# Kernel tuning notes

Measured on AMD Instinct MI355X. Metric: run time of the kernel, lower is better.

## Reference

```python
import jax, jax.numpy as jnp
import numpy as np

N = 10000
E = 320000
DIN = 256
HID = 64
HEADS = 4
LAT = 32
NEG_SLOPE = 0.2


def _layer_params(key, din, heads, out_c):
    ks = jax.random.split(key, 6)
    s_in = 1.0 / np.sqrt(din)
    return dict(
        Wl=jax.random.normal(ks[0], (din, heads * out_c), jnp.float32) * s_in,
        bl=jnp.zeros((heads * out_c,), jnp.float32),
        Wr=jax.random.normal(ks[1], (din, heads * out_c), jnp.float32) * s_in,
        br=jnp.zeros((heads * out_c,), jnp.float32),
        att=jax.random.normal(ks[2], (heads, out_c), jnp.float32) * (1.0 / np.sqrt(out_c)),
        bo=jnp.zeros((heads * out_c,), jnp.float32),
    )


def setup_inputs() -> dict:
    key = jax.random.key(0)
    ks = jax.random.split(key, 8)
    inp = {
        "x": jax.random.normal(ks[0], (N, DIN), jnp.float32),
        "edge_index": jax.random.randint(ks[1], (2, E), 0, N, jnp.int64 if jax.config.jax_enable_x64 else jnp.int32),
        "eps": jax.random.normal(ks[2], (N, LAT), jnp.float32),
    }
    p0 = _layer_params(ks[3], DIN, HEADS, HID)
    p1 = _layer_params(ks[4], HID * HEADS, HEADS, HID)
    pmu = _layer_params(ks[5], HID * HEADS, 1, LAT)
    plv = _layer_params(ks[6], HID * HEADS, 1, LAT)
    for tag, p in (("l0", p0), ("l1", p1), ("mu", pmu), ("lv", plv)):
        for k, v in p.items():
            inp[f"{k}_{tag}"] = v
    return inp


def _gatv2(h, src, dst, Wl, bl, Wr, br, att, bo, heads, out_c, concat):
    # GATv2: e_ij = att . LeakyReLU(lin_l(x_j) + lin_r(x_i)), softmax over j for each i,
    # out_i = sum_j alpha_ij * lin_l(x_j). src = j (source), dst = i (target).
    xl = (h @ Wl + bl).reshape(-1, heads, out_c)  # [N,H,C]
    xr = (h @ Wr + br).reshape(-1, heads, out_c)
    e = jax.nn.leaky_relu(xl[src] + xr[dst], NEG_SLOPE)  # [E,H,C]
    score = jnp.einsum('ehc,hc->eh', e, att)             # [E,H]
    smax = jax.ops.segment_max(score, dst, num_segments=N)
    ex = jnp.exp(score - smax[dst])
    denom = jax.ops.segment_sum(ex, dst, num_segments=N)
    alpha = ex / (denom[dst] + 1e-16)                    # [E,H]
    out = jax.ops.segment_sum(alpha[:, :, None] * xl[src], dst, num_segments=N)  # [N,H,C]
    out = out.reshape(N, heads * out_c) if concat else out.mean(axis=1)
    return out + bo


def reference(x, edge_index, eps,
              Wl_l0, bl_l0, Wr_l0, br_l0, att_l0, bo_l0,
              Wl_l1, bl_l1, Wr_l1, br_l1, att_l1, bo_l1,
              Wl_mu, bl_mu, Wr_mu, br_mu, att_mu, bo_mu,
              Wl_lv, bl_lv, Wr_lv, br_lv, att_lv, bo_lv):
    loop = jnp.arange(N, dtype=edge_index.dtype)
    src = jnp.concatenate([edge_index[0], loop])  # add self-loops (PyG default)
    dst = jnp.concatenate([edge_index[1], loop])
    h = jax.nn.elu(_gatv2(x, src, dst, Wl_l0, bl_l0, Wr_l0, br_l0, att_l0, bo_l0, HEADS, HID, True))
    h = jax.nn.elu(_gatv2(h, src, dst, Wl_l1, bl_l1, Wr_l1, br_l1, att_l1, bo_l1, HEADS, HID, True))
    mu = _gatv2(h, src, dst, Wl_mu, bl_mu, Wr_mu, br_mu, att_mu, bo_mu, 1, LAT, False)
    log_var = _gatv2(h, src, dst, Wl_lv, bl_lv, Wr_lv, br_lv, att_lv, bo_lv, 1, LAT, False)
    z = mu + eps * jnp.exp(0.5 * log_var)  # reparameterize (training mode)
    adj_recon = z @ z.T                    # [N,N] dense decode
    return (adj_recon, mu, log_var)
```

## Files before the change

### kernel.cpp

```cpp
#include <hip/hip_runtime.h>
#include <hip/hip_bf16.h>
#include <math.h>

constexpr int Nn  = 10000;
constexpr int Ed  = 320000;
constexpr int DIN = 256;
constexpr float NEG = 0.2f;

constexpr size_t OFF_XL  = 0;
constexpr size_t OFF_XR  = 2560000;
constexpr size_t OFF_H   = 5120000;
constexpr size_t OFF_XSL = 7680000;
constexpr size_t OFF_XSR = 8320000;
constexpr size_t OFF_WLC = 8960000;
constexpr size_t OFF_WRC = 8976384;
constexpr size_t OFF_BLC = 8992768;
constexpr size_t OFF_BRC = 8992832;
constexpr size_t OFF_ATT = 8992896;
constexpr size_t OFF_BOC = 8992960;
constexpr size_t OFF_INT = 9000000;
constexpr int I_DEG = 0;
constexpr int I_ROW = 16384;
constexpr int I_CUR = 32768;
constexpr int I_CSR = 49152;
static_assert(OFF_INT + (I_CSR + Ed + Nn + 4) < 100000000, "scratch fits in adj region");

__device__ __forceinline__ unsigned short f2bf(float x) {
    unsigned int u = __float_as_uint(x);
    unsigned int r = (u + 0x7FFFu + ((u >> 16) & 1u)) >> 16;
    return (unsigned short)r;
}
__device__ __forceinline__ float bf2f(unsigned short b) {
    return __uint_as_float(((unsigned int)b) << 16);
}

typedef short bf16x8 __attribute__((ext_vector_type(8)));
typedef float f32x4  __attribute__((ext_vector_type(4)));

__global__ void k_init_deg(int* deg, int n) {
    int i = blockIdx.x * blockDim.x + threadIdx.x;
    if (i < n) deg[i] = 1;
}

__global__ void k_count(const int* __restrict__ dst, int* deg, int e) {
    int i = blockIdx.x * blockDim.x + threadIdx.x;
    if (i < e) atomicAdd(&deg[dst[i]], 1);
}

__global__ void k_scan(const int* __restrict__ deg, int* row_ptr, int* cursor, int n) {
    __shared__ int sums[256];
    int t = threadIdx.x;
    int chunk = (n + 255) / 256;
    int start = t * chunk, end = min(start + chunk, n);
    int s = 0;
    for (int i = start; i < end; ++i) s += deg[i];
    sums[t] = s;
    __syncthreads();
    for (int off = 1; off < 256; off <<= 1) {
        int v = (t >= off) ? sums[t - off] : 0;
        __syncthreads();
        sums[t] += v;
        __syncthreads();
    }
    int run = sums[t] - s;
    for (int i = start; i < end; ++i) { row_ptr[i] = run; cursor[i] = run; run += deg[i]; }
    if (t == 255) row_ptr[n] = sums[255];
}

__global__ void k_scatter(const int* __restrict__ src, const int* __restrict__ dst,
                          int* cursor, int* csr, int e, int n) {
    int i = blockIdx.x * blockDim.x + threadIdx.x;
    if (i < e) {
        int d = dst[i];
        int pos = atomicAdd(&cursor[d], 1);
        csr[pos] = src[i];
    } else if (i < e + n) {
        int v = i - e;
        int pos = atomicAdd(&cursor[v], 1);
        csr[pos] = v;
    }
}

template <typename OT>
__global__ __launch_bounds__(256) void k_gemm(const float* __restrict__ A,
                                              const float* __restrict__ W,
                                              const float* __restrict__ bias,
                                              OT* __restrict__ out,
                                              int M, int Ncols) {
    constexpr int K = 256;
    __shared__ float As[32][68];
    __shared__ float Ws[32][64];
    int tid = threadIdx.x;
    int tx = tid & 15, ty = tid >> 4;
    int m0 = blockIdx.x * 64, n0 = blockIdx.y * 64;
    float acc[4][4] = {};
    int am = tid >> 2, akb = (tid & 3) * 8;
    int wk = tid >> 3, wnb = (tid & 7) * 8;
    const bool arow_ok = (m0 + am) < M;
    const float* Aptr = A + (size_t)(m0 + am) * K + akb;
    const float* Wptr = W + (size_t)wk * Ncols + n0 + wnb;

    for (int k0 = 0; k0 < K; k0 += 32) {
        float4 a0 = {0, 0, 0, 0}, a1 = {0, 0, 0, 0};
        if (arow_ok) {
            a0 = *(const float4*)(Aptr + k0);
            a1 = *(const float4*)(Aptr + k0 + 4);
        }
        float4 w0 = *(const float4*)(Wptr + (size_t)k0 * Ncols);
        float4 w1 = *(const float4*)(Wptr + (size_t)k0 * Ncols + 4);
        __syncthreads();
        As[akb + 0][am] = a0.x; As[akb + 1][am] = a0.y; As[akb + 2][am] = a0.z; As[akb + 3][am] = a0.w;
        As[akb + 4][am] = a1.x; As[akb + 5][am] = a1.y; As[akb + 6][am] = a1.z; As[akb + 7][am] = a1.w;
        *(float4*)&Ws[wk][wnb] = w0;
        *(float4*)&Ws[wk][wnb + 4] = w1;
        __syncthreads();
        #pragma unroll
        for (int k = 0; k < 32; ++k) {
            float4 a = *(const float4*)&As[k][ty * 4];
            float4 b = *(const float4*)&Ws[k][tx * 4];
            float av[4] = {a.x, a.y, a.z, a.w};
            float bv[4] = {b.x, b.y, b.z, b.w};
            #pragma unroll
            for (int i2 = 0; i2 < 4; ++i2)
                #pragma unroll
                for (int j2 = 0; j2 < 4; ++j2)
                    acc[i2][j2] = fmaf(av[i2], bv[j2], acc[i2][j2]);
        }
    }
    #pragma unroll
    for (int i2 = 0; i2 < 4; ++i2) {
        int row = m0 + ty * 4 + i2;
        if (row < M) {
            int col = n0 + tx * 4;
            float o0 = acc[i2][0] + bias[col + 0];
            float o1 = acc[i2][1] + bias[col + 1];
            float o2 = acc[i2][2] + bias[col + 2];
            float o3 = acc[i2][3] + bias[col + 3];
            if constexpr (sizeof(OT) == 4) {
                float4 o = {o0, o1, o2, o3};
                *(float4*)&out[(size_t)row * Ncols + col] = o;
            } else {
                ushort4 s;
                s.x = f2bf(o0); s.y = f2bf(o1); s.z = f2bf(o2); s.w = f2bf(o3);
                *(ushort4*)&out[(size_t)row * Ncols + col] = s;
            }
        }
    }
}

__device__ __forceinline__ float lrelu(float x) { return x > 0.f ? x : NEG * x; }

template <bool DO_ELU>
__global__ __launch_bounds__(256) void k_gat4(const unsigned short* __restrict__ xl,
                                              const float* __restrict__ xr,
                                              const float* __restrict__ att,
                                              const float* __restrict__ bo,
                                              const int* __restrict__ row_ptr,
                                              const int* __restrict__ csr,
                                              float* __restrict__ out, int n) {
    int lane = threadIdx.x & 63;
    int node = (blockIdx.x * blockDim.x + threadIdx.x) >> 6;
    if (node >= n) return;
    int f = lane * 4;
    float4 xrr  = *(const float4*)&xr[(size_t)node * 256 + f];
    float4 attr = *(const float4*)&att[f];
    float m = -INFINITY, d = 0.f;
    float4 acc = {0.f, 0.f, 0.f, 0.f};

    int e0 = row_ptr[node], e1 = row_ptr[node + 1];
    int e = e0;
    for (; e + 1 < e1; e += 2) {
        int ja = csr[e], jb = csr[e + 1];
        ushort4 ua = *(const ushort4*)&xl[(size_t)ja * 256 + f];
        ushort4 ub = *(const ushort4*)&xl[(size_t)jb * 256 + f];
        float4 va = {bf2f(ua.x), bf2f(ua.y), bf2f(ua.z), bf2f(ua.w)};
        float4 vb = {bf2f(ub.x), bf2f(ub.y), bf2f(ub.z), bf2f(ub.w)};
        float ta = attr.x * lrelu(va.x + xrr.x) + attr.y * lrelu(va.y + xrr.y)
                 + attr.z * lrelu(va.z + xrr.z) + attr.w * lrelu(va.w + xrr.w);
        float tb = attr.x * lrelu(vb.x + xrr.x) + attr.y * lrelu(vb.y + xrr.y)
                 + attr.z * lrelu(vb.z + xrr.z) + attr.w * lrelu(vb.w + xrr.w);
        #pragma unroll
        for (int mask = 1; mask <= 8; mask <<= 1) {
            ta += __shfl_xor(ta, mask, 64);
            tb += __shfl_xor(tb, mask, 64);
        }
        float mn = fmaxf(m, fmaxf(ta, tb));
        float sc = __expf(m - mn);
        float pa = __expf(ta - mn), pb = __expf(tb - mn);
        d = d * sc + pa + pb;
        acc.x = acc.x * sc + pa * va.x + pb * vb.x;
        acc.y = acc.y * sc + pa * va.y + pb * vb.y;
        acc.z = acc.z * sc + pa * va.z + pb * vb.z;
        acc.w = acc.w * sc + pa * va.w + pb * vb.w;
        m = mn;
    }
    if (e < e1) {
        int j = csr[e];
        ushort4 u = *(const ushort4*)&xl[(size_t)j * 256 + f];
        float4 v = {bf2f(u.x), bf2f(u.y), bf2f(u.z), bf2f(u.w)};
        float t = attr.x * lrelu(v.x + xrr.x) + attr.y * lrelu(v.y + xrr.y)
                + attr.z * lrelu(v.z + xrr.z) + attr.w * lrelu(v.w + xrr.w);
        #pragma unroll
        for (int mask = 1; mask <= 8; mask <<= 1) t += __shfl_xor(t, mask, 64);
        float mn = fmaxf(m, t);
        float sc = __expf(m - mn), p = __expf(t - mn);
        d = d * sc + p;
        acc.x = acc.x * sc + p * v.x;
        acc.y = acc.y * sc + p * v.y;
        acc.z = acc.z * sc + p * v.z;
        acc.w = acc.w * sc + p * v.w;
        m = mn;
    }
    float inv = 1.f / (d + 1e-16f);
    float4 bo4 = *(const float4*)&bo[f];
    float4 o;
    o.x = acc.x * inv + bo4.x;
    o.y = acc.y * inv + bo4.y;
    o.z = acc.z * inv + bo4.z;
    o.w = acc.w * inv + bo4.w;
    if (DO_ELU) {
        o.x = o.x > 0.f ? o.x : expm1f(o.x);
        o.y = o.y > 0.f ? o.y : expm1f(o.y);
        o.z = o.z > 0.f ? o.z : expm1f(o.z);
        o.w = o.w > 0.f ? o.w : expm1f(o.w);
    }
    *(float4*)&out[(size_t)node * 256 + f] = o;
}

template <int H, int C, bool DO_ELU, bool SPLIT>
__global__ __launch_bounds__(256) void k_gat(const unsigned short* __restrict__ xl,
                                             const float* __restrict__ xr,
                                             const float* __restrict__ att,
                                             const float* __restrict__ bo,
                                             const int* __restrict__ row_ptr,
                                             const int* __restrict__ csr,
                                             float* __restrict__ out0,
                                             float* __restrict__ out1, int n) {
    constexpr int F = H * C;
    constexpr int R = F / 64;
    int lane = threadIdx.x & 63;
    int node = (blockIdx.x * blockDim.x + threadIdx.x) >> 6;
    if (node >= n) return;

    float xrr[R], attr[R], m[R], d[R], acc[R];
    #pragma unroll
    for (int r = 0; r < R; ++r) {
        xrr[r]  = xr[(size_t)node * F + r * 64 + lane];
        attr[r] = att[r * 64 + lane];
        m[r] = -INFINITY;
        d[r] = 0.f;
        acc[r] = 0.f;
    }
    int e0 = row_ptr[node], e1 = row_ptr[node + 1];
    for (int e = e0; e < e1; ++e) {
        int j = csr[e];
        float v[R], s[R];
        #pragma unroll
        for (int r = 0; r < R; ++r) {
            v[r] = bf2f(xl[(size_t)j * F + r * 64 + lane]);
            float t = v[r] + xrr[r];
            t = (t > 0.f) ? t : NEG * t;
            t *= attr[r];
            #pragma unroll
            for (int mask = C / 2; mask >= 1; mask >>= 1)
                t += __shfl_xor(t, mask, 64);
            s[r] = t;
        }
        #pragma unroll
        for (int r = 0; r < R; ++r) {
            if (s[r] > m[r]) {
                float sc = __expf(m[r] - s[r]);
                d[r] *= sc; acc[r] *= sc; m[r] = s[r];
            }
            float p = __expf(s[r] - m[r]);
            d[r] += p;
            acc[r] = fmaf(p, v[r], acc[r]);
        }
    }
    #pragma unroll
    for (int r = 0; r < R; ++r) {
        float o = acc[r] / (d[r] + 1e-16f) + bo[r * 64 + lane];
        if (DO_ELU) o = (o > 0.f) ? o : expm1f(o);
        if (SPLIT) {
            int f = r * 64 + lane;
            int h = f / C, c = f % C;
            float* op = (h == 0) ? out0 : out1;
            op[(size_t)node * C + c] = o;
        } else {
            out0[(size_t)node * F + r * 64 + lane] = o;
        }
    }
}

__global__ void k_cat(const float* __restrict__ Wlmu, const float* __restrict__ Wllv,
                      const float* __restrict__ Wrmu, const float* __restrict__ Wrlv,
                      const float* __restrict__ blmu, const float* __restrict__ bllv,
                      const float* __restrict__ brmu, const float* __restrict__ brlv,
                      const float* __restrict__ attmu, const float* __restrict__ attlv,
                      const float* __restrict__ bomu, const float* __restrict__ bolv,
                      float* WLC, float* WRC, float* BLC, float* BRC, float* ATTC, float* BOC) {
    int i = blockIdx.x * blockDim.x + threadIdx.x;
    if (i < 256 * 64) {
        int k = i >> 6, c = i & 63;
        WLC[i] = (c < 32) ? Wlmu[k * 32 + c] : Wllv[k * 32 + c - 32];
        WRC[i] = (c < 32) ? Wrmu[k * 32 + c] : Wrlv[k * 32 + c - 32];
    }
    if (i < 64) {
        BLC[i]  = (i < 32) ? blmu[i]  : bllv[i - 32];
        BRC[i]  = (i < 32) ? brmu[i]  : brlv[i - 32];
        ATTC[i] = (i < 32) ? attmu[i] : attlv[i - 32];
        BOC[i]  = (i < 32) ? bomu[i]  : bolv[i - 32];
    }
}

__global__ void k_z2(const float* __restrict__ mu, const float* __restrict__ lv,
                     const float* __restrict__ eps,
                     unsigned short* __restrict__ zhi,
                     unsigned short* __restrict__ zlo, int n) {
    int i = blockIdx.x * blockDim.x + threadIdx.x;
    if (i < n * 8) {
        float4 m4 = ((const float4*)mu)[i];
        float4 l4 = ((const float4*)lv)[i];
        float4 e4 = ((const float4*)eps)[i];
        float zv[4];
        zv[0] = m4.x + e4.x * __expf(0.5f * l4.x);
        zv[1] = m4.y + e4.y * __expf(0.5f * l4.y);
        zv[2] = m4.z + e4.z * __expf(0.5f * l4.z);
        zv[3] = m4.w + e4.w * __expf(0.5f * l4.w);
        ushort4 h, lo;
        h.x = f2bf(zv[0]); lo.x = f2bf(zv[0] - bf2f(h.x));
        h.y = f2bf(zv[1]); lo.y = f2bf(zv[1] - bf2f(h.y));
        h.z = f2bf(zv[2]); lo.z = f2bf(zv[2] - bf2f(h.z));
        h.w = f2bf(zv[3]); lo.w = f2bf(zv[3] - bf2f(h.w));
        *(ushort4*)&zhi[(size_t)i * 4] = h;
        *(ushort4*)&zlo[(size_t)i * 4] = lo;
    }
}

constexpr int JTM = 25;

__global__ __launch_bounds__(256) void k_adjm(const unsigned short* __restrict__ zhi,
                                              const unsigned short* __restrict__ zlo,
                                              float* __restrict__ adj, int n) {
    int wave  = threadIdx.x >> 6;
    int l     = threadIdx.x & 63;
    int strip = blockIdx.y * 4 + wave;
    if (strip * 16 >= n) return;
    int i0   = strip * 16;
    int arow = i0 + (l & 15);
    int koff = (l >> 4) * 8;
    bf16x8 a_hi = *(const bf16x8*)(zhi + (size_t)arow * 32 + koff);
    bf16x8 a_lo = *(const bf16x8*)(zlo + (size_t)arow * 32 + koff);
    int crow = i0 + (l >> 4) * 4;

    for (int t = 0; t < JTM; ++t) {
        int j0   = (blockIdx.x * JTM + t) * 16;
        int brow = j0 + (l & 15);
        bf16x8 b_hi = *(const bf16x8*)(zhi + (size_t)brow * 32 + koff);
        bf16x8 b_lo = *(const bf16x8*)(zlo + (size_t)brow * 32 + koff);
        f32x4 acc = {0.f, 0.f, 0.f, 0.f};
        acc = __builtin_amdgcn_mfma_f32_16x16x32_bf16(a_hi, b_hi, acc, 0, 0, 0);
        acc = __builtin_amdgcn_mfma_f32_16x16x32_bf16(a_hi, b_lo, acc, 0, 0, 0);
        acc = __builtin_amdgcn_mfma_f32_16x16x32_bf16(a_lo, b_hi, acc, 0, 0, 0);
        size_t base = (size_t)crow * n + j0 + (l & 15);
        adj[base]                 = acc[0];
        adj[base + (size_t)n]     = acc[1];
        adj[base + (size_t)n * 2] = acc[2];
        adj[base + (size_t)n * 3] = acc[3];
    }
}

constexpr int JT = 8;
__global__ __launch_bounds__(256) void k_adj_fb(const float* __restrict__ mu,
                                                const float* __restrict__ lv,
                                                const float* __restrict__ eps,
                                                float* __restrict__ adj, int n) {
    __shared__ float Zi[32][68];
    __shared__ float Zj[32][68];
    int tid = threadIdx.x;
    int tx = tid & 15, ty = tid >> 4;
    int i0 = blockIdx.y * 64;
    int r = tid >> 2, kq = (tid & 3) * 8;

    auto load8 = [&](int row, float4& a, float4& b) {
        a = make_float4(0.f, 0.f, 0.f, 0.f);
        b = make_float4(0.f, 0.f, 0.f, 0.f);
        if (row < n) {
            float4 m0 = *(const float4*)&mu[row * 32 + kq];
            float4 l0 = *(const float4*)&lv[row * 32 + kq];
            float4 e0 = *(const float4*)&eps[row * 32 + kq];
            float4 m1 = *(const float4*)&mu[row * 32 + kq + 4];
            float4 l1 = *(const float4*)&lv[row * 32 + kq + 4];
            float4 e1 = *(const float4*)&eps[row * 32 + kq + 4];
            a.x = m0.x + e0.x * __expf(0.5f * l0.x);
            a.y = m0.y + e0.y * __expf(0.5f * l0.y);
            a.z = m0.z + e0.z * __expf(0.5f * l0.z);
            a.w = m0.w + e0.w * __expf(0.5f * l0.w);
            b.x = m1.x + e1.x * __expf(0.5f * l1.x);
            b.y = m1.y + e1.y * __expf(0.5f * l1.y);
            b.z = m1.z + e1.z * __expf(0.5f * l1.z);
            b.w = m1.w + e1.w * __expf(0.5f * l1.w);
        }
    };

    {
        float4 a, b;
        load8(i0 + r, a, b);
        Zi[kq + 0][r] = a.x; Zi[kq + 1][r] = a.y; Zi[kq + 2][r] = a.z; Zi[kq + 3][r] = a.w;
        Zi[kq + 4][r] = b.x; Zi[kq + 5][r] = b.y; Zi[kq + 6][r] = b.z; Zi[kq + 7][r] = b.w;
    }
    __syncthreads();
    float4 af[32];
    #pragma unroll
    for (int k = 0; k < 32; ++k) af[k] = *(const float4*)&Zi[k][ty * 4];

    for (int jt = 0; jt < JT; ++jt) {
        int j0 = (blockIdx.x * JT + jt) * 64;
        if (j0 >= n) break;
        {
            float4 a, b;
            load8(j0 + r, a, b);
            __syncthreads();
            Zj[kq + 0][r] = a.x; Zj[kq + 1][r] = a.y; Zj[kq + 2][r] = a.z; Zj[kq + 3][r] = a.w;
            Zj[kq + 4][r] = b.x; Zj[kq + 5][r] = b.y; Zj[kq + 6][r] = b.z; Zj[kq + 7][r] = b.w;
            __syncthreads();
        }
        float acc[4][4] = {};
        #pragma unroll
        for (int k = 0; k < 32; ++k) {
            float4 b = *(const float4*)&Zj[k][tx * 4];
            float av[4] = {af[k].x, af[k].y, af[k].z, af[k].w};
            float bv[4] = {b.x, b.y, b.z, b.w};
            #pragma unroll
            for (int i2 = 0; i2 < 4; ++i2)
                #pragma unroll
                for (int j2 = 0; j2 < 4; ++j2)
                    acc[i2][j2] = fmaf(av[i2], bv[j2], acc[i2][j2]);
        }
        int col = j0 + tx * 4;
        if (col < n) {
            #pragma unroll
            for (int i2 = 0; i2 < 4; ++i2) {
                int row = i0 + ty * 4 + i2;
                if (row < n) {
                    float4 o = {acc[i2][0], acc[i2][1], acc[i2][2], acc[i2][3]};
                    *(float4*)&adj[(size_t)row * n + col] = o;
                }
            }
        }
    }
}

extern "C" void kernel_launch(void* const* d_in, const int* in_sizes, int n_in,
                              void* d_out, int out_size, void* d_ws, size_t ws_size,
                              hipStream_t stream) {
    const float* x      = (const float*)d_in[0];
    const int*   edges  = (const int*)d_in[1];
    const float* eps    = (const float*)d_in[2];
    const float* Wl0 = (const float*)d_in[3];
    const float* bl0 = (const float*)d_in[4];
    const float* Wr0 = (const float*)d_in[5];
    const float* br0 = (const float*)d_in[6];
    const float* at0 = (const float*)d_in[7];
    const float* bo0 = (const float*)d_in[8];
    const float* Wl1 = (const float*)d_in[9];
    const float* bl1 = (const float*)d_in[10];
    const float* Wr1 = (const float*)d_in[11];
    const float* br1 = (const float*)d_in[12];
    const float* at1 = (const float*)d_in[13];
    const float* bo1 = (const float*)d_in[14];
    const float* Wlmu = (const float*)d_in[15];
    const float* blmu = (const float*)d_in[16];
    const float* Wrmu = (const float*)d_in[17];
    const float* brmu = (const float*)d_in[18];
    const float* atmu = (const float*)d_in[19];
    const float* bomu = (const float*)d_in[20];
    const float* Wllv = (const float*)d_in[21];
    const float* bllv = (const float*)d_in[22];
    const float* Wrlv = (const float*)d_in[23];
    const float* brlv = (const float*)d_in[24];
    const float* atlv = (const float*)d_in[25];
    const float* bolv = (const float*)d_in[26];

    float* base   = (float*)d_out;
    float* adj    = base;
    float* mu_out = base + (size_t)Nn * Nn;
    float* lv_out = mu_out + (size_t)Nn * 32;

    unsigned short* XLB  = (unsigned short*)(base + OFF_XL);
    float* XR  = base + OFF_XR;
    float* H   = base + OFF_H;
    unsigned short* XSLB = (unsigned short*)(base + OFF_XSL);
    float* XSR = base + OFF_XSR;
    float* WLC = base + OFF_WLC;
    float* WRC = base + OFF_WRC;
    float* BLC = base + OFF_BLC;
    float* BRC = base + OFF_BRC;
    float* ATT = base + OFF_ATT;
    float* BOC = base + OFF_BOC;
    int* ib  = (int*)(base + OFF_INT);
    int* deg = ib + I_DEG;
    int* row = ib + I_ROW;
    int* cur = ib + I_CUR;
    int* csr = ib + I_CSR;
    const int* srcp = edges;
    const int* dstp = edges + Ed;

    k_init_deg<<<(Nn + 255) / 256, 256, 0, stream>>>(deg, Nn);
    k_count<<<(Ed + 255) / 256, 256, 0, stream>>>(dstp, deg, Ed);
    k_scan<<<1, 256, 0, stream>>>(deg, row, cur, Nn);
    k_scatter<<<(Ed + Nn + 255) / 256, 256, 0, stream>>>(srcp, dstp, cur, csr, Ed, Nn);

    dim3 g4(157, 4), g1(157, 1);
    k_gemm<unsigned short><<<g4, 256, 0, stream>>>(x, Wl0, bl0, XLB, Nn, 256);
    k_gemm<float><<<g4, 256, 0, stream>>>(x, Wr0, br0, XR, Nn, 256);
    k_gat4<true><<<2500, 256, 0, stream>>>(XLB, XR, at0, bo0, row, csr, H, Nn);
    k_gemm<unsigned short><<<g4, 256, 0, stream>>>(H, Wl1, bl1, XLB, Nn, 256);
    k_gemm<float><<<g4, 256, 0, stream>>>(H, Wr1, br1, XR, Nn, 256);
    k_gat4<true><<<2500, 256, 0, stream>>>(XLB, XR, at1, bo1, row, csr, H, Nn);
    k_cat<<<64, 256, 0, stream>>>(Wlmu, Wllv, Wrmu, Wrlv, blmu, bllv, brmu, brlv,
                                  atmu, atlv, bomu, bolv, WLC, WRC, BLC, BRC, ATT, BOC);
    k_gemm<unsigned short><<<g1, 256, 0, stream>>>(H, WLC, BLC, XSLB, Nn, 64);
    k_gemm<float><<<g1, 256, 0, stream>>>(H, WRC, BRC, XSR, Nn, 64);
    k_gat<2, 32, false, true><<<2500, 256, 0, stream>>>(XSLB, XSR, ATT, BOC, row, csr, mu_out, lv_out, Nn);

    size_t need = (size_t)Nn * 32 * 2 * sizeof(unsigned short);
    if (ws_size >= need) {
        unsigned short* zhi = (unsigned short*)d_ws;
        unsigned short* zlo = zhi + (size_t)Nn * 32;
        k_z2<<<(Nn * 8 + 255) / 256, 256, 0, stream>>>(mu_out, lv_out, eps, zhi, zlo, Nn);
        dim3 ga(25, 157);
        k_adjm<<<ga, 256, 0, stream>>>(zhi, zlo, adj, Nn);
    } else {
        dim3 ga(20, 157);
        k_adj_fb<<<ga, 256, 0, stream>>>(mu_out, lv_out, eps, adj, Nn);
    }
}
```

Baseline: 431.6 us.

## Fuse lin_l/lin_r GEMMs per layer and fold reparameterization into final GAT

Merges the two separate GEMMs for lin_l and lin_r into one kernel that loads each A tile once and accumulates against both weight matrices. The z reparameterization (mu + eps*exp(0.5*logvar), split into bf16 hi/lo) is moved into the final GAT kernel, which removes the k_z2 launch and its re-read of mu and log_var. This saves repeated activation reads and three kernel launches, at the cost of double the register accumulators and more shared memory in the GEMM, which may reduce occupancy.

```diff
diff --git a/kernel.cpp b/kernel.cpp
--- a/kernel.cpp
+++ b/kernel.cpp
@@ -81,24 +81,29 @@
     }
 }
 
-template <typename OT>
-__global__ __launch_bounds__(256) void k_gemm(const float* __restrict__ A,
-                                              const float* __restrict__ W,
-                                              const float* __restrict__ bias,
-                                              OT* __restrict__ out,
-                                              int M, int Ncols) {
+template <int NC>
+__global__ __launch_bounds__(256) void k_gemm2(const float* __restrict__ A,
+                                               const float* __restrict__ WL,
+                                               const float* __restrict__ biasL,
+                                               unsigned short* __restrict__ outL,
+                                               const float* __restrict__ WR,
+                                               const float* __restrict__ biasR,
+                                               float* __restrict__ outR,
+                                               int M) {
     constexpr int K = 256;
     __shared__ float As[32][68];
-    __shared__ float Ws[32][64];
+    __shared__ float WsL[32][64];
+    __shared__ float WsR[32][64];
     int tid = threadIdx.x;
     int tx = tid & 15, ty = tid >> 4;
     int m0 = blockIdx.x * 64, n0 = blockIdx.y * 64;
-    float acc[4][4] = {};
+    float accL[4][4] = {}, accR[4][4] = {};
     int am = tid >> 2, akb = (tid & 3) * 8;
     int wk = tid >> 3, wnb = (tid & 7) * 8;
     const bool arow_ok = (m0 + am) < M;
-    const float* Aptr = A + (size_t)(m0 + am) * K + akb;
-    const float* Wptr = W + (size_t)wk * Ncols + n0 + wnb;
+    const float* Aptr  = A  + (size_t)(m0 + am) * K + akb;
+    const float* WLptr = WL + (size_t)wk * NC + n0 + wnb;
+    const float* WRptr = WR + (size_t)wk * NC + n0 + wnb;
 
     for (int k0 = 0; k0 < K; k0 += 32) {
         float4 a0 = {0, 0, 0, 0}, a1 = {0, 0, 0, 0};
@@ -106,25 +111,33 @@
             a0 = *(const float4*)(Aptr + k0);
             a1 = *(const float4*)(Aptr + k0 + 4);
         }
-        float4 w0 = *(const float4*)(Wptr + (size_t)k0 * Ncols);
-        float4 w1 = *(const float4*)(Wptr + (size_t)k0 * Ncols + 4);
+        float4 wl0 = *(const float4*)(WLptr + (size_t)k0 * NC);
+        float4 wl1 = *(const float4*)(WLptr + (size_t)k0 * NC + 4);
+        float4 wr0 = *(const float4*)(WRptr + (size_t)k0 * NC);
+        float4 wr1 = *(const float4*)(WRptr + (size_t)k0 * NC + 4);
         __syncthreads();
         As[akb + 0][am] = a0.x; As[akb + 1][am] = a0.y; As[akb + 2][am] = a0.z; As[akb + 3][am] = a0.w;
         As[akb + 4][am] = a1.x; As[akb + 5][am] = a1.y; As[akb + 6][am] = a1.z; As[akb + 7][am] = a1.w;
-        *(float4*)&Ws[wk][wnb] = w0;
-        *(float4*)&Ws[wk][wnb + 4] = w1;
+        *(float4*)&WsL[wk][wnb]     = wl0;
+        *(float4*)&WsL[wk][wnb + 4] = wl1;
+        *(float4*)&WsR[wk][wnb]     = wr0;
+        *(float4*)&WsR[wk][wnb + 4] = wr1;
         __syncthreads();
         #pragma unroll
         for (int k = 0; k < 32; ++k) {
-            float4 a = *(const float4*)&As[k][ty * 4];
-            float4 b = *(const float4*)&Ws[k][tx * 4];
-            float av[4] = {a.x, a.y, a.z, a.w};
-            float bv[4] = {b.x, b.y, b.z, b.w};
+            float4 a  = *(const float4*)&As[k][ty * 4];
+            float4 bl = *(const float4*)&WsL[k][tx * 4];
+            float4 br = *(const float4*)&WsR[k][tx * 4];
+            float av[4]  = {a.x, a.y, a.z, a.w};
+            float blv[4] = {bl.x, bl.y, bl.z, bl.w};
+            float brv[4] = {br.x, br.y, br.z, br.w};
             #pragma unroll
             for (int i2 = 0; i2 < 4; ++i2)
                 #pragma unroll
-                for (int j2 = 0; j2 < 4; ++j2)
-                    acc[i2][j2] = fmaf(av[i2], bv[j2], acc[i2][j2]);
+                for (int j2 = 0; j2 < 4; ++j2) {
+                    accL[i2][j2] = fmaf(av[i2], blv[j2], accL[i2][j2]);
+                    accR[i2][j2] = fmaf(av[i2], brv[j2], accR[i2][j2]);
+                }
         }
     }
     #pragma unroll
@@ -132,18 +145,18 @@
         int row = m0 + ty * 4 + i2;
         if (row < M) {
             int col = n0 + tx * 4;
-            float o0 = acc[i2][0] + bias[col + 0];
-            float o1 = acc[i2][1] + bias[col + 1];
-            float o2 = acc[i2][2] + bias[col + 2];
-            float o3 = acc[i2][3] + bias[col + 3];
-            if constexpr (sizeof(OT) == 4) {
-                float4 o = {o0, o1, o2, o3};
-                *(float4*)&out[(size_t)row * Ncols + col] = o;
-            } else {
-                ushort4 s;
-                s.x = f2bf(o0); s.y = f2bf(o1); s.z = f2bf(o2); s.w = f2bf(o3);
-                *(ushort4*)&out[(size_t)row * Ncols + col] = s;
-            }
+            ushort4 s;
+            s.x = f2bf(accL[i2][0] + biasL[col + 0]);
+            s.y = f2bf(accL[i2][1] + biasL[col + 1]);
+            s.z = f2bf(accL[i2][2] + biasL[col + 2]);
+            s.w = f2bf(accL[i2][3] + biasL[col + 3]);
+            *(ushort4*)&outL[(size_t)row * NC + col] = s;
+            float4 o;
+            o.x = accR[i2][0] + biasR[col + 0];
+            o.y = accR[i2][1] + biasR[col + 1];
+            o.z = accR[i2][2] + biasR[col + 2];
+            o.w = accR[i2][3] + biasR[col + 3];
+            *(float4*)&outR[(size_t)row * NC + col] = o;
         }
     }
 }
@@ -227,68 +240,54 @@
     *(float4*)&out[(size_t)node * 256 + f] = o;
 }
 
-template <int H, int C, bool DO_ELU, bool SPLIT>
-__global__ __launch_bounds__(256) void k_gat(const unsigned short* __restrict__ xl,
-                                             const float* __restrict__ xr,
-                                             const float* __restrict__ att,
-                                             const float* __restrict__ bo,
-                                             const int* __restrict__ row_ptr,
-                                             const int* __restrict__ csr,
-                                             float* __restrict__ out0,
-                                             float* __restrict__ out1, int n) {
-    constexpr int F = H * C;
-    constexpr int R = F / 64;
+__global__ __launch_bounds__(256) void k_gatz(const unsigned short* __restrict__ xl,
+                                              const float* __restrict__ xr,
+                                              const float* __restrict__ att,
+                                              const float* __restrict__ bo,
+                                              const int* __restrict__ row_ptr,
+                                              const int* __restrict__ csr,
+                                              const float* __restrict__ eps,
+                                              float* __restrict__ out0,
+                                              float* __restrict__ out1,
+                                              unsigned short* __restrict__ zhi,
+                                              unsigned short* __restrict__ zlo, int n) {
+    constexpr int C = 32;
     int lane = threadIdx.x & 63;
     int node = (blockIdx.x * blockDim.x + threadIdx.x) >> 6;
     if (node >= n) return;
 
-    float xrr[R], attr[R], m[R], d[R], acc[R];
-    #pragma unroll
-    for (int r = 0; r < R; ++r) {
-        xrr[r]  = xr[(size_t)node * F + r * 64 + lane];
-        attr[r] = att[r * 64 + lane];
-        m[r] = -INFINITY;
-        d[r] = 0.f;
-        acc[r] = 0.f;
-    }
+    float xrr  = xr[(size_t)node * 64 + lane];
+    float attr = att[lane];
+    float m = -INFINITY, d = 0.f, acc = 0.f;
+
     int e0 = row_ptr[node], e1 = row_ptr[node + 1];
     for (int e = e0; e < e1; ++e) {
         int j = csr[e];
-        float v[R], s[R];
+        float v = bf2f(xl[(size_t)j * 64 + lane]);
+        float t = v + xrr;
+        t = (t > 0.f) ? t : NEG * t;
+        t *= attr;
         #pragma unroll
-        for (int r = 0; r < R; ++r) {
-            v[r] = bf2f(xl[(size_t)j * F + r * 64 + lane]);
-            float t = v[r] + xrr[r];
-            t = (t > 0.f) ? t : NEG * t;
-            t *= attr[r];
-            #pragma unroll
-            for (int mask = C / 2; mask >= 1; mask >>= 1)
-                t += __shfl_xor(t, mask, 64);
-            s[r] = t;
-        }
-        #pragma unroll
-        for (int r = 0; r < R; ++r) {
-            if (s[r] > m[r]) {
-                float sc = __expf(m[r] - s[r]);
-                d[r] *= sc; acc[r] *= sc; m[r] = s[r];
-            }
-            float p = __expf(s[r] - m[r]);
-            d[r] += p;
-            acc[r] = fmaf(p, v[r], acc[r]);
-        }
-    }
-    #pragma unroll
-    for (int r = 0; r < R; ++r) {
-        float o = acc[r] / (d[r] + 1e-16f) + bo[r * 64 + lane];
-        if (DO_ELU) o = (o > 0.f) ? o : expm1f(o);
-        if (SPLIT) {
-            int f = r * 64 + lane;
-            int h = f / C, c = f % C;
-            float* op = (h == 0) ? out0 : out1;
-            op[(size_t)node * C + c] = o;
-        } else {
-            out0[(size_t)node * F + r * 64 + lane] = o;
-        }
+        for (int mask = C / 2; mask >= 1; mask >>= 1)
+            t += __shfl_xor(t, mask, 64);
+        if (t > m) {
+            float sc = __expf(m - t);
+            d *= sc; acc *= sc; m = t;
+        }
+        float p = __expf(t - m);
+        d += p;
+        acc = fmaf(p, v, acc);
+    }
+    float o = acc / (d + 1e-16f) + bo[lane];
+    int c = lane & 31;
+    float* op = (lane < 32) ? out0 : out1;
+    op[(size_t)node * C + c] = o;
+    float lvv = __shfl(o, lane + 32, 64);
+    if (zhi != nullptr && lane < 32) {
+        float zc = o + eps[(size_t)node * 32 + lane] * __expf(0.5f * lvv);
+        unsigned short h = f2bf(zc);
+        zhi[(size_t)node * 32 + lane] = h;
+        zlo[(size_t)node * 32 + lane] = f2bf(zc - bf2f(h));
     }
 }
 
@@ -310,30 +309,6 @@
         BRC[i]  = (i < 32) ? brmu[i]  : brlv[i - 32];
         ATTC[i] = (i < 32) ? attmu[i] : attlv[i - 32];
         BOC[i]  = (i < 32) ? bomu[i]  : bolv[i - 32];
-    }
-}
-
-__global__ void k_z2(const float* __restrict__ mu, const float* __restrict__ lv,
-                     const float* __restrict__ eps,
-                     unsigned short* __restrict__ zhi,
-                     unsigned short* __restrict__ zlo, int n) {
-    int i = blockIdx.x * blockDim.x + threadIdx.x;
-    if (i < n * 8) {
-        float4 m4 = ((const float4*)mu)[i];
-        float4 l4 = ((const float4*)lv)[i];
-        float4 e4 = ((const float4*)eps)[i];
-        float zv[4];
-        zv[0] = m4.x + e4.x * __expf(0.5f * l4.x);
-        zv[1] = m4.y + e4.y * __expf(0.5f * l4.y);
-        zv[2] = m4.z + e4.z * __expf(0.5f * l4.z);
-        zv[3] = m4.w + e4.w * __expf(0.5f * l4.w);
-        ushort4 h, lo;
-        h.x = f2bf(zv[0]); lo.x = f2bf(zv[0] - bf2f(h.x));
-        h.y = f2bf(zv[1]); lo.y = f2bf(zv[1] - bf2f(h.y));
-        h.z = f2bf(zv[2]); lo.z = f2bf(zv[2] - bf2f(h.z));
-        h.w = f2bf(zv[3]); lo.w = f2bf(zv[3] - bf2f(h.w));
-        *(ushort4*)&zhi[(size_t)i * 4] = h;
-        *(ushort4*)&zlo[(size_t)i * 4] = lo;
     }
 }
 
@@ -506,29 +481,27 @@
     const int* srcp = edges;
     const int* dstp = edges + Ed;
 
+    size_t need = (size_t)Nn * 32 * 2 * sizeof(unsigned short);
+    unsigned short* zhi = (ws_size >= need) ? (unsigned short*)d_ws : nullptr;
+    unsigned short* zlo = zhi ? zhi + (size_t)Nn * 32 : nullptr;
+
     k_init_deg<<<(Nn + 255) / 256, 256, 0, stream>>>(deg, Nn);
     k_count<<<(Ed + 255) / 256, 256, 0, stream>>>(dstp, deg, Ed);
     k_scan<<<1, 256, 0, stream>>>(deg, row, cur, Nn);
     k_scatter<<<(Ed + Nn + 255) / 256, 256, 0, stream>>>(srcp, dstp, cur, csr, Ed, Nn);
 
     dim3 g4(157, 4), g1(157, 1);
-    k_gemm<unsigned short><<<g4, 256, 0, stream>>>(x, Wl0, bl0, XLB, Nn, 256);
-    k_gemm<float><<<g4, 256, 0, stream>>>(x, Wr0, br0, XR, Nn, 256);
+    k_gemm2<256><<<g4, 256, 0, stream>>>(x, Wl0, bl0, XLB, Wr0, br0, XR, Nn);
     k_gat4<true><<<2500, 256, 0, stream>>>(XLB, XR, at0, bo0, row, csr, H, Nn);
-    k_gemm<unsigned short><<<g4, 256, 0, stream>>>(H, Wl1, bl1, XLB, Nn, 256);
-    k_gemm<float><<<g4, 256, 0, stream>>>(H, Wr1, br1, XR, Nn, 256);
+    k_gemm2<256><<<g4, 256, 0, stream>>>(H, Wl1, bl1, XLB, Wr1, br1, XR, Nn);
     k_gat4<true><<<2500, 256, 0, stream>>>(XLB, XR, at1, bo1, row, csr, H, Nn);
     k_cat<<<64, 256, 0, stream>>>(Wlmu, Wllv, Wrmu, Wrlv, blmu, bllv, brmu, brlv,
                                   atmu, atlv, bomu, bolv, WLC, WRC, BLC, BRC, ATT, BOC);
-    k_gemm<unsigned short><<<g1, 256, 0, stream>>>(H, WLC, BLC, XSLB, Nn, 64);
-    k_gemm<float><<<g1, 256, 0, stream>>>(H, WRC, BRC, XSR, Nn, 64);
-    k_gat<2, 32, false, true><<<2500, 256, 0, stream>>>(XSLB, XSR, ATT, BOC, row, csr, mu_out, lv_out, Nn);
-
-    size_t need = (size_t)Nn * 32 * 2 * sizeof(unsigned short);
-    if (ws_size >= need) {
-        unsigned short* zhi = (unsigned short*)d_ws;
-        unsigned short* zlo = zhi + (size_t)Nn * 32;
-        k_z2<<<(Nn * 8 + 255) / 256, 256, 0, stream>>>(mu_out, lv_out, eps, zhi, zlo, Nn);
+    k_gemm2<64><<<g1, 256, 0, stream>>>(H, WLC, BLC, XSLB, WRC, BRC, XSR, Nn);
+    k_gatz<<<2500, 256, 0, stream>>>(XSLB, XSR, ATT, BOC, row, csr, eps,
+                                     mu_out, lv_out, zhi, zlo, Nn);
+
+    if (zhi) {
         dim3 ga(25, 157);
         k_adjm<<<ga, 256, 0, stream>>>(zhi, zlo, adj, Nn);
     } else {
```

After: 408.5 us. 1.06x faster.
